# Optimization experiments

Hardware: AMD Instinct MI355X
Metric: run time of the kernel (lower is better)

Reference implementation:

```python
import jax, jax.numpy as jnp
import numpy as np

B, D, E, TOP_K = 16384, 2048, 8, 2


def setup_inputs() -> dict:
    key = jax.random.key(0)
    ks = jax.random.split(key, 5)
    scale = 1.0 / np.sqrt(D)
    x = jax.random.normal(ks[0], (B, D), dtype=jnp.float32)
    # expert Linear(D, D) weights/biases, stacked over experts
    expert_w = jax.random.uniform(ks[1], (E, D, D), minval=-scale, maxval=scale, dtype=jnp.float32)
    expert_b = jax.random.uniform(ks[2], (E, D), minval=-scale, maxval=scale, dtype=jnp.float32)
    # gate Linear(D, E)
    gate_w = jax.random.uniform(ks[3], (D, E), minval=-scale, maxval=scale, dtype=jnp.float32)
    gate_b = jax.random.uniform(ks[4], (E,), minval=-scale, maxval=scale, dtype=jnp.float32)
    return {"x": x, "expert_w": expert_w, "expert_b": expert_b, "gate_w": gate_w, "gate_b": gate_b}


def reference(x, expert_w, expert_b, gate_w, gate_b):
    # gate logits: (B, E)
    logits = x @ gate_w + gate_b
    topk_logits, topk_idx = jax.lax.top_k(logits, TOP_K)          # (B, K)
    topk_weights = jax.nn.softmax(topk_logits, axis=-1)           # (B, K)
    # dense: compute every expert for every token (faithful to original)
    expert_outputs = jax.nn.relu(
        jnp.einsum("bd,edf->bef", x, expert_w) + expert_b[None, :, :]
    )                                                             # (B, E, D); dropout is identity in eval mode
    # gather the top-k experts per token
    selected = jnp.take_along_axis(expert_outputs, topk_idx[:, :, None], axis=1)  # (B, K, D)
    out = jnp.sum(selected * topk_weights[:, :, None], axis=1)    # (B, D)
    return out
```

## Files before the change

### kernel.cpp

```cpp
#include <hip/hip_runtime.h>
#include <hip/hip_bf16.h>
#include <math.h>

#define NB 16384
#define DD 2048
#define NE 8
#define TM 128
#define TN 128
#define BK 64
#define NKT (DD / BK)
#define MT_PER_PASS (NB / TM + NE)
#define NT_TILES (DD / TN)
#define GEMM_GRID (MT_PER_PASS * NT_TILES)
#define BPX (GEMM_GRID / 8)

typedef float f32x4 __attribute__((ext_vector_type(4)));
typedef short bf16x8 __attribute__((ext_vector_type(8)));

__device__ __forceinline__ short f2bf(float f) {
  union { float f; unsigned u; } v; v.f = f;
  unsigned r = (v.u + 0x7FFFu + ((v.u >> 16) & 1u)) >> 16;
  return (short)r;
}

__device__ __forceinline__ void gload16(const void* g, void* l) {
  __builtin_amdgcn_global_load_lds((const __attribute__((address_space(1))) void*)g,
                                   (__attribute__((address_space(3))) void*)l,
                                   16, 0, 0);
}

__global__ void conv_wT(const float* __restrict__ w, short* __restrict__ wt) {
  __shared__ float tile[64][68];
  int bid = blockIdx.x;
  int e = bid >> 10;
  int tt = bid & 1023;
  int d0 = (tt >> 5) << 6;
  int f0 = (tt & 31) << 6;
  const float* we = w + (size_t)e * DD * DD;
  int t = threadIdx.x;
  int col = (t & 15) << 2;
#pragma unroll
  for (int p = 0; p < 4; ++p) {
    int dl = (t >> 4) + p * 16;
    f32x4 v = *(const f32x4*)(we + (size_t)(d0 + dl) * DD + f0 + col);
    *(f32x4*)&tile[dl][col] = v;
  }
  __syncthreads();
  int fl = t >> 2;
  int ds = (t & 3) << 4;
  short tmp[16];
#pragma unroll
  for (int j = 0; j < 16; ++j) tmp[j] = f2bf(tile[ds + j][fl]);
  short* dst = wt + (size_t)e * DD * DD + (size_t)(f0 + fl) * DD + d0 + ds;
  *(bf16x8*)dst = *(const bf16x8*)tmp;
  *(bf16x8*)(dst + 8) = *(const bf16x8*)(tmp + 8);
}

__global__ void gate_conv(const float* __restrict__ x, const float* __restrict__ gw,
                          const float* __restrict__ gb, short* __restrict__ xb,
                          int* __restrict__ ridx, float* __restrict__ rw) {
  int wid = threadIdx.x >> 6;
  int lane = threadIdx.x & 63;
  int b = blockIdx.x * 4 + wid;
  const float* xr = x + (size_t)b * DD;
  short* xbr = xb + (size_t)b * DD;
  double acc[8];
#pragma unroll
  for (int e = 0; e < 8; ++e) acc[e] = 0.0;
#pragma unroll
  for (int it = 0; it < 4; ++it) {
    int d8 = (it * 64 + lane) * 8;
    f32x4 a = *(const f32x4*)(xr + d8);
    f32x4 c = *(const f32x4*)(xr + d8 + 4);
    bf16x8 o;
    o[0] = f2bf(a[0]); o[1] = f2bf(a[1]); o[2] = f2bf(a[2]); o[3] = f2bf(a[3]);
    o[4] = f2bf(c[0]); o[5] = f2bf(c[1]); o[6] = f2bf(c[2]); o[7] = f2bf(c[3]);
    *(bf16x8*)(xbr + d8) = o;
#pragma unroll
    for (int j = 0; j < 8; ++j) {
      float xv = (j < 4) ? a[j] : c[j - 4];
      double xd = (double)xv;
      f32x4 g0 = *(const f32x4*)(gw + (size_t)(d8 + j) * 8);
      f32x4 g1 = *(const f32x4*)(gw + (size_t)(d8 + j) * 8 + 4);
      acc[0] += xd * g0[0]; acc[1] += xd * g0[1];
      acc[2] += xd * g0[2]; acc[3] += xd * g0[3];
      acc[4] += xd * g1[0]; acc[5] += xd * g1[1];
      acc[6] += xd * g1[2]; acc[7] += xd * g1[3];
    }
  }
#pragma unroll
  for (int off = 32; off > 0; off >>= 1) {
#pragma unroll
    for (int e = 0; e < 8; ++e) acc[e] += __shfl_down(acc[e], off);
  }
  if (lane == 0) {
    double l[8];
#pragma unroll
    for (int e = 0; e < 8; ++e) l[e] = acc[e] + (double)gb[e];
    int i0 = 0;
#pragma unroll
    for (int e = 1; e < 8; ++e) if (l[e] > l[i0]) i0 = e;
    int i1 = (i0 == 0) ? 1 : 0;
#pragma unroll
    for (int e = 0; e < 8; ++e) if (e != i0 && l[e] > l[i1]) i1 = e;
    double z = exp(l[i1] - l[i0]);
    float w0 = (float)(1.0 / (1.0 + z));
    float w1 = (float)(z / (1.0 + z));
    ridx[2 * b] = i0; ridx[2 * b + 1] = i1;
    rw[2 * b] = w0;   rw[2 * b + 1] = w1;
  }
}

__global__ void hist_tok(const int* __restrict__ ridx, int* __restrict__ partials) {
  __shared__ int h[16];
  int t = threadIdx.x;
  if (t < 16) h[t] = 0;
  __syncthreads();
  int t0 = blockIdx.x * 512;
  for (int i = t; i < 512; i += 256) {
    int tok = t0 + i;
    atomicAdd(&h[ridx[2 * tok]], 1);
    atomicAdd(&h[8 + ridx[2 * tok + 1]], 1);
  }
  __syncthreads();
  if (t < 16) partials[blockIdx.x * 16 + t] = h[t];
}

__global__ void scan_small(const int* __restrict__ partials, int* __restrict__ base,
                           int* __restrict__ cnts, int* __restrict__ offs) {
  __shared__ int c[16], o[16];
  int j = threadIdx.x;
  if (j < 16) {
    int s = 0;
    for (int b = 0; b < 32; ++b) s += partials[b * 16 + j];
    c[j] = s; cnts[j] = s;
  }
  __syncthreads();
  if (j < 2) {
    int a = 0;
    for (int e = 0; e < 8; ++e) { o[j * 8 + e] = a; a += c[j * 8 + e]; }
  }
  __syncthreads();
  if (j < 16) {
    int r = o[j];
    offs[j] = o[j];
    for (int b = 0; b < 32; ++b) { base[b * 16 + j] = r; r += partials[b * 16 + j]; }
  }
}

__global__ void scatter_tok(const int* __restrict__ ridx, const float* __restrict__ rw,
                            const int* __restrict__ base,
                            int* __restrict__ lists0, float* __restrict__ elw0,
                            int* __restrict__ lists1, float* __restrict__ elw1) {
  __shared__ int h[16];
  int t = threadIdx.x;
  if (t < 16) h[t] = 0;
  __syncthreads();
  int t0 = blockIdx.x * 512;
  const int* bb = base + blockIdx.x * 16;
  for (int i = t; i < 512; i += 256) {
    int tok = t0 + i;
    int e0 = ridx[2 * tok], e1 = ridx[2 * tok + 1];
    int r0 = atomicAdd(&h[e0], 1);
    int r1 = atomicAdd(&h[8 + e1], 1);
    int p0 = bb[e0] + r0;
    int p1 = bb[8 + e1] + r1;
    lists0[p0] = tok; elw0[p0] = rw[2 * tok];
    lists1[p1] = tok; elw1[p1] = rw[2 * tok + 1];
  }
}

template <int ADD>
__global__ __launch_bounds__(256, 4)
void moe_gemm(const short* __restrict__ xb, const short* __restrict__ wt,
              const float* __restrict__ eb, const int* __restrict__ cnts,
              const int* __restrict__ offs, const int* __restrict__ lists,
              const float* __restrict__ elw, float* __restrict__ out) {
  __shared__ short As[TM * BK];
  __shared__ short Bs[TN * BK];

  int bid = blockIdx.x;
  int swz = (bid & 7) * BPX + (bid >> 3);
  int mt = swz % MT_PER_PASS;
  int nt = swz / MT_PER_PASS;

  int e = 0, cnt = 0;
  for (; e < NE; ++e) {
    cnt = cnts[e];
    int te = (cnt + TM - 1) >> 7;
    if (mt < te) break;
    mt -= te;
  }
  if (e >= NE) return;

  int m0 = mt * TM;
  int n0 = nt * TN;
  int off_e = offs[e];
  int tid = threadIdx.x;
  int lane = tid & 63, wid = tid >> 6;
  int wr = wid >> 1, wc = wid & 1;

  int trow = tid >> 3;
  int scol = ((tid & 7) ^ (trow & 7)) << 3;
  int tok[4];
#pragma unroll
  for (int l = 0; l < 4; ++l) {
    int gr = m0 + l * 32 + trow;
    tok[l] = lists[off_e + ((gr < cnt) ? gr : (cnt - 1))];
  }
  const short* bbase = wt + ((size_t)e * DD + (size_t)(n0 + trow)) * DD + scol;

  int lane15 = lane & 15;
  int csw0 = (((lane >> 4)    ) ^ (lane & 7)) << 3;
  int csw1 = (((lane >> 4) + 4) ^ (lane & 7)) << 3;
  int arow = (wr * 64 + lane15) * 64;
  int brow = (wc * 64 + lane15) * 64;

  f32x4 acc[4][4];
#pragma unroll
  for (int i = 0; i < 4; ++i)
#pragma unroll
    for (int j = 0; j < 4; ++j) acc[i][j] = (f32x4){0.f, 0.f, 0.f, 0.f};

#pragma unroll 1
  for (int kt = 0; kt < NKT; ++kt) {
    int ko = kt * BK + scol;
#pragma unroll
    for (int l = 0; l < 4; ++l) {
      gload16(xb + ((size_t)tok[l] << 11) + ko, &As[l * 2048 + tid * 8]);
      gload16(bbase + (size_t)(l * 32) * DD + kt * BK, &Bs[l * 2048 + tid * 8]);
    }
    __syncthreads();
    bf16x8 bfr[4][2];
#pragma unroll
    for (int j = 0; j < 4; ++j) {
      int br = brow + j * 16 * 64;
      bfr[j][0] = *(const bf16x8*)&Bs[br + csw0];
      bfr[j][1] = *(const bf16x8*)&Bs[br + csw1];
    }
#pragma unroll
    for (int i = 0; i < 4; ++i) {
      int ar = arow + i * 16 * 64;
      bf16x8 a0 = *(const bf16x8*)&As[ar + csw0];
      bf16x8 a1 = *(const bf16x8*)&As[ar + csw1];
#pragma unroll
      for (int j = 0; j < 4; ++j) {
        acc[i][j] = __builtin_amdgcn_mfma_f32_16x16x32_bf16(a0, bfr[j][0], acc[i][j], 0, 0, 0);
        acc[i][j] = __builtin_amdgcn_mfma_f32_16x16x32_bf16(a1, bfr[j][1], acc[i][j], 0, 0, 0);
      }
    }
    __syncthreads();
  }

  int r0 = (lane >> 4) << 2;
#pragma unroll
  for (int i = 0; i < 4; ++i) {
    int mloc = wr * 64 + i * 16 + r0;
#pragma unroll
    for (int r = 0; r < 4; ++r) {
      int gr = m0 + mloc + r;
      if (gr >= cnt) continue;
      int tokr = lists[off_e + gr];
      float wgt = elw[off_e + gr];
      float* orow = out + (size_t)tokr * DD;
#pragma unroll
      for (int j = 0; j < 4; ++j) {
        int n = n0 + wc * 64 + j * 16 + lane15;
        float v = acc[i][j][r] + eb[e * DD + n];
        v = fmaxf(v, 0.f) * wgt;
        if (ADD) v += __builtin_nontemporal_load(&orow[n]);
        __builtin_nontemporal_store(v, &orow[n]);
      }
    }
  }
}

extern "C" void kernel_launch(void* const* d_in, const int* in_sizes, int n_in,
                              void* d_out, int out_size, void* d_ws, size_t ws_size,
                              hipStream_t stream) {
  const float* x   = (const float*)d_in[0];
  const float* ewt = (const float*)d_in[1];
  const float* eb  = (const float*)d_in[2];
  const float* gw  = (const float*)d_in[3];
  const float* gb  = (const float*)d_in[4];
  float* out = (float*)d_out;

  char* ws = (char*)d_ws;
  short* xb      = (short*)(ws);
  short* wt      = (short*)(ws + 67108864);
  int*   ridx    = (int*)  (ws + 134217728);
  float* rw      = (float*)(ws + 134348800);
  int*   lists0  = (int*)  (ws + 134479872);
  float* elw0    = (float*)(ws + 134545408);
  int*   lists1  = (int*)  (ws + 134610944);
  float* elw1    = (float*)(ws + 134676480);
  int*   partials= (int*)  (ws + 134742016);
  int*   base    = (int*)  (ws + 134744064);
  int*   cnts    = (int*)  (ws + 134746112);
  int*   offs    = (int*)  (ws + 134746176);

  conv_wT<<<NE * 32 * 32, 256, 0, stream>>>(ewt, wt);
  gate_conv<<<NB / 4, 256, 0, stream>>>(x, gw, gb, xb, ridx, rw);
  hist_tok<<<32, 256, 0, stream>>>(ridx, partials);
  scan_small<<<1, 64, 0, stream>>>(partials, base, cnts, offs);
  scatter_tok<<<32, 256, 0, stream>>>(ridx, rw, base, lists0, elw0, lists1, elw1);
  moe_gemm<0><<<GEMM_GRID, 256, 0, stream>>>(xb, wt, eb, cnts,     offs,     lists0, elw0, out);
  moe_gemm<1><<<GEMM_GRID, 256, 0, stream>>>(xb, wt, eb, cnts + 8, offs + 8, lists1, elw1, out);
}
```

Before: 618.7 us.

## Double-buffer LDS tiles with BK=32 to overlap global loads and MFMA

Halves the K tile to 32 and adds two LDS buffers so the next tile's global-to-LDS loads are issued before the current tile's MFMAs. This drops one barrier per iteration and is meant to hide global load latency. The swizzle pattern and per-thread load mapping are reworked for the 32-wide tile. The cost is twice as many iterations with less MFMA work each, and some risk of read/write hazards since only one barrier separates the buffers.

```diff
diff --git a/kernel.cpp b/kernel.cpp
--- a/kernel.cpp
+++ b/kernel.cpp
@@ -7,8 +7,8 @@
 #define NE 8
 #define TM 128
 #define TN 128
-#define BK 64
-#define NKT (DD / BK)
+#define BK 32
+#define NKT2 (DD / BK)
 #define MT_PER_PASS (NB / TM + NE)
 #define NT_TILES (DD / TN)
 #define GEMM_GRID (MT_PER_PASS * NT_TILES)
@@ -176,8 +176,8 @@
               const float* __restrict__ eb, const int* __restrict__ cnts,
               const int* __restrict__ offs, const int* __restrict__ lists,
               const float* __restrict__ elw, float* __restrict__ out) {
-  __shared__ short As[TM * BK];
-  __shared__ short Bs[TN * BK];
+  __shared__ short As[2 * 4096];
+  __shared__ short Bs[2 * 4096];
 
   int bid = blockIdx.x;
   int swz = (bid & 7) * BPX + (bid >> 3);
@@ -200,21 +200,23 @@
   int lane = tid & 63, wid = tid >> 6;
   int wr = wid >> 1, wc = wid & 1;
 
-  int trow = tid >> 3;
-  int scol = ((tid & 7) ^ (trow & 7)) << 3;
-  int tok[4];
-#pragma unroll
-  for (int l = 0; l < 4; ++l) {
-    int gr = m0 + l * 32 + trow;
-    tok[l] = lists[off_e + ((gr < cnt) ? gr : (cnt - 1))];
-  }
-  const short* bbase = wt + ((size_t)e * DD + (size_t)(n0 + trow)) * DD + scol;
+  int trow = tid >> 2;
+  int scolw = (((tid & 3) ^ ((tid >> 3) & 3)) << 3);
+  const short* asrc[2];
+  const short* bsrc[2];
+#pragma unroll
+  for (int l = 0; l < 2; ++l) {
+    int r = l * 64 + trow;
+    int gr = m0 + r;
+    int tok = lists[off_e + ((gr < cnt) ? gr : (cnt - 1))];
+    asrc[l] = xb + ((size_t)tok << 11) + scolw;
+    bsrc[l] = wt + ((size_t)e * DD + (size_t)(n0 + r)) * DD + scolw;
+  }
 
   int lane15 = lane & 15;
-  int csw0 = (((lane >> 4)    ) ^ (lane & 7)) << 3;
-  int csw1 = (((lane >> 4) + 4) ^ (lane & 7)) << 3;
-  int arow = (wr * 64 + lane15) * 64;
-  int brow = (wc * 64 + lane15) * 64;
+  int csw = (((lane >> 4) ^ ((lane15 >> 1) & 3)) << 3);
+  int arow = (wr * 64 + lane15) * 32;
+  int brow = (wc * 64 + lane15) * 32;
 
   f32x4 acc[4][4];
 #pragma unroll
@@ -222,35 +224,33 @@
 #pragma unroll
     for (int j = 0; j < 4; ++j) acc[i][j] = (f32x4){0.f, 0.f, 0.f, 0.f};
 
-#pragma unroll 1
-  for (int kt = 0; kt < NKT; ++kt) {
-    int ko = kt * BK + scol;
-#pragma unroll
-    for (int l = 0; l < 4; ++l) {
-      gload16(xb + ((size_t)tok[l] << 11) + ko, &As[l * 2048 + tid * 8]);
-      gload16(bbase + (size_t)(l * 32) * DD + kt * BK, &Bs[l * 2048 + tid * 8]);
+#define STAGE(buf, kt) {                                                        \
+  _Pragma("unroll") for (int l = 0; l < 2; ++l) {                               \
+    gload16(asrc[l] + (size_t)(kt) * BK, &As[(buf)*4096 + l*2048 + tid*8]);     \
+    gload16(bsrc[l] + (size_t)(kt) * BK, &Bs[(buf)*4096 + l*2048 + tid*8]);     \
+  } }
+
+  STAGE(0, 0);
+  __syncthreads();
+
+#pragma unroll 2
+  for (int kt = 0; kt < NKT2; ++kt) {
+    int cur = kt & 1;
+    if (kt + 1 < NKT2) STAGE(cur ^ 1, kt + 1);
+    bf16x8 bfr[4];
+#pragma unroll
+    for (int j = 0; j < 4; ++j)
+      bfr[j] = *(const bf16x8*)&Bs[cur * 4096 + brow + j * 512 + csw];
+#pragma unroll
+    for (int i = 0; i < 4; ++i) {
+      bf16x8 a0 = *(const bf16x8*)&As[cur * 4096 + arow + i * 512 + csw];
+#pragma unroll
+      for (int j = 0; j < 4; ++j)
+        acc[i][j] = __builtin_amdgcn_mfma_f32_16x16x32_bf16(a0, bfr[j], acc[i][j], 0, 0, 0);
     }
     __syncthreads();
-    bf16x8 bfr[4][2];
-#pragma unroll
-    for (int j = 0; j < 4; ++j) {
-      int br = brow + j * 16 * 64;
-      bfr[j][0] = *(const bf16x8*)&Bs[br + csw0];
-      bfr[j][1] = *(const bf16x8*)&Bs[br + csw1];
-    }
-#pragma unroll
-    for (int i = 0; i < 4; ++i) {
-      int ar = arow + i * 16 * 64;
-      bf16x8 a0 = *(const bf16x8*)&As[ar + csw0];
-      bf16x8 a1 = *(const bf16x8*)&As[ar + csw1];
-#pragma unroll
-      for (int j = 0; j < 4; ++j) {
-        acc[i][j] = __builtin_amdgcn_mfma_f32_16x16x32_bf16(a0, bfr[j][0], acc[i][j], 0, 0, 0);
-        acc[i][j] = __builtin_amdgcn_mfma_f32_16x16x32_bf16(a1, bfr[j][1], acc[i][j], 0, 0, 0);
-      }
-    }
-    __syncthreads();
-  }
+  }
+#undef STAGE
 
   int r0 = (lane >> 4) << 2;
 #pragma unroll
```

New measurement: 703.1 us. 13.6% more time.
